# Kernel tuning notes

Hardware: AMD Instinct MI355X
Metric: run time of the kernel (lower is better)

The kernel has to match this reference:

```python
import jax, jax.numpy as jnp
import numpy as np


def _chamfer(xyz1, xyz2):
    # xyz1: [B,N,3], xyz2: [B,M,3]
    sq1 = jnp.sum(xyz1 * xyz1, axis=-1)               # [B,N]
    sq2 = jnp.sum(xyz2 * xyz2, axis=-1)               # [B,M]
    cross = jnp.einsum('bnc,bmc->bnm', xyz1, xyz2)    # [B,N,M]
    d = sq1[:, :, None] + sq2[:, None, :] - 2.0 * cross  # [B,N,M] squared dists
    dist1 = jnp.min(d, axis=2)                        # [B,N]
    idx1 = jnp.argmin(d, axis=2).astype(jnp.int32)    # [B,N]
    dist2 = jnp.min(d, axis=1)                        # [B,M]
    idx2 = jnp.argmin(d, axis=1).astype(jnp.int32)    # [B,M]
    return dist1, dist2, idx1, idx2


def setup_inputs() -> dict:
    key = jax.random.key(0)
    k1, k2 = jax.random.split(key)
    B, N, M = 2, 8192, 8192
    xyz1 = jax.random.normal(k1, (B, N, 3), dtype=jnp.float32)
    xyz2 = jax.random.normal(k2, (B, M, 3), dtype=jnp.float32)
    return {"xyz1": xyz1, "xyz2": xyz2}


def reference(xyz1, xyz2):
    # Matches ChamferDistanceFunction.forward: returns (dist1, dist2, idx1, idx2)
    # with SQUARED distances, as in the CUDA kernel.
    return _chamfer(xyz1, xyz2)
```

## Files before the change

kernel.cpp:

```cpp
#include <hip/hip_runtime.h>
#include <stdint.h>

#define TPB   256
#define Q     4
#define CHUNK 128

typedef unsigned long long ull;

__device__ __forceinline__ uint32_t enc_f32(float f) {
    uint32_t u = __float_as_uint(f);
    return (u & 0x80000000u) ? ~u : (u | 0x80000000u);
}

__device__ __forceinline__ float sq_np(float x, float y, float z) {
    return __fadd_rn(__fadd_rn(__fmul_rn(x, x), __fmul_rn(y, y)), __fmul_rn(z, z));
}

__global__ void __launch_bounds__(TPB) chamfer_pass1(
    const float* __restrict__ xyz1, const float* __restrict__ xyz2,
    ull* __restrict__ P, int B, int N, int M)
{
    __shared__ float4 pts[CHUNK];

    int z   = blockIdx.z;
    int dir = z / B;
    int b   = z - dir * B;

    const float* src; const float* dst; int Ns, Nd; size_t ebase;
    if (dir == 0) { src = xyz1; dst = xyz2; Ns = N; Nd = M; ebase = (size_t)b * N; }
    else          { src = xyz2; dst = xyz1; Ns = M; Nd = N; ebase = (size_t)B * N + (size_t)b * M; }

    int t     = threadIdx.x;
    int mbase = blockIdx.y * CHUNK;

    for (int i = t; i < CHUNK; i += TPB) {
        int m = mbase + i;
        if (m < Nd) {
            const float* p = dst + ((size_t)b * Nd + m) * 3;
            float x = p[0], y = p[1], zz = p[2];
            pts[i] = make_float4(x, y, zz, sq_np(x, y, zz));
        } else {
            pts[i] = make_float4(0.f, 0.f, 0.f, 3.0e38f);
        }
    }

    int n0 = blockIdx.x * (TPB * Q) + t;
    float qx[Q], qy[Q], qz[Q], qs[Q];
    #pragma unroll
    for (int k = 0; k < Q; ++k) {
        int n = n0 + k * TPB;
        if (n < Ns) {
            const float* p = src + ((size_t)b * Ns + n) * 3;
            qx[k] = p[0]; qy[k] = p[1]; qz[k] = p[2];
            qs[k] = sq_np(qx[k], qy[k], qz[k]);
        } else { qx[k] = 0.f; qy[k] = 0.f; qz[k] = 0.f; qs[k] = 0.f; }
    }
    __syncthreads();

    float best[Q];
    int   bidx[Q];
    #pragma unroll
    for (int k = 0; k < Q; ++k) { best[k] = 3.4e38f; bidx[k] = 0; }

    #pragma unroll 2
    for (int i = 0; i < CHUNK; i += 2) {
        float4 c0 = pts[i];
        float4 c1 = pts[i + 1];
        #pragma unroll
        for (int k = 0; k < Q; ++k) {
            float cr0 = __fadd_rn(__fadd_rn(__fmul_rn(qx[k], c0.x), __fmul_rn(qy[k], c0.y)),
                                  __fmul_rn(qz[k], c0.z));
            float d0  = fmaf(-2.0f, cr0, __fadd_rn(qs[k], c0.w));
            float cr1 = __fadd_rn(__fadd_rn(__fmul_rn(qx[k], c1.x), __fmul_rn(qy[k], c1.y)),
                                  __fmul_rn(qz[k], c1.z));
            float d1  = fmaf(-2.0f, cr1, __fadd_rn(qs[k], c1.w));
            float nb  = fminf(best[k], fminf(d0, d1));
            int   sel = (d0 == nb) ? (mbase + i) : (mbase + i + 1);
            bidx[k]   = (best[k] == nb) ? bidx[k] : sel;
            best[k]   = nb;
        }
    }

    #pragma unroll
    for (int k = 0; k < Q; ++k) {
        int n = n0 + k * TPB;
        if (n < Ns) {
            ull key = ((ull)enc_f32(best[k]) << 32) | (unsigned int)bidx[k];
            atomicMin(&P[ebase + n], key);
        }
    }
}

__global__ void __launch_bounds__(256) chamfer_unpack(
    const ull* __restrict__ P, float* __restrict__ out, int entries)
{
    int e = blockIdx.x * 256 + threadIdx.x;
    if (e < entries) {
        ull pk = P[e];
        uint32_t encu = (uint32_t)(pk >> 32);
        uint32_t bits = (encu & 0x80000000u) ? (encu & 0x7FFFFFFFu) : ~encu;
        out[e]           = __uint_as_float(bits);
        out[entries + e] = (float)(uint32_t)pk;
    }
}

__global__ void __launch_bounds__(1024) chamfer_unpack_inplace(float* __restrict__ out)
{
    const int entries = 32768;
    const ull* P = (const ull*)out;
    int t = threadIdx.x;
    ull v[32];
    #pragma unroll
    for (int k = 0; k < 32; ++k) v[k] = P[t + k * 1024];
    __syncthreads();
    #pragma unroll
    for (int k = 0; k < 32; ++k) {
        int e = t + k * 1024;
        ull pk = v[k];
        uint32_t encu = (uint32_t)(pk >> 32);
        uint32_t bits = (encu & 0x80000000u) ? (encu & 0x7FFFFFFFu) : ~encu;
        out[e]           = __uint_as_float(bits);
        out[entries + e] = (float)(uint32_t)pk;
    }
}

extern "C" void kernel_launch(void* const* d_in, const int* in_sizes, int n_in,
                              void* d_out, int out_size, void* d_ws, size_t ws_size,
                              hipStream_t stream) {
    const float* xyz1 = (const float*)d_in[0];
    const float* xyz2 = (const float*)d_in[1];
    const int B = 2;
    const int N = in_sizes[0] / (B * 3);
    const int M = in_sizes[1] / (B * 3);

    float* out = (float*)d_out;
    const int entries = B * N + B * M;
    const size_t pbytes = (size_t)entries * sizeof(ull);

    int maxP = (N > M) ? N : M;
    dim3 grid((maxP + TPB * Q - 1) / (TPB * Q), (maxP + CHUNK - 1) / CHUNK, 2 * B);

    if (ws_size >= pbytes) {
        ull* P = (ull*)d_ws;
        hipMemsetAsync(d_ws, 0xFF, pbytes, stream);
        chamfer_pass1<<<grid, TPB, 0, stream>>>(xyz1, xyz2, P, B, N, M);
        chamfer_unpack<<<(entries + 255) / 256, 256, 0, stream>>>(P, out, entries);
    } else {
        ull* P = (ull*)d_out;
        hipMemsetAsync(d_out, 0xFF, pbytes, stream);
        chamfer_pass1<<<grid, TPB, 0, stream>>>(xyz1, xyz2, P, B, N, M);
        if (entries == 32768) {
            chamfer_unpack_inplace<<<1, 1024, 0, stream>>>(out);
        } else {
            chamfer_unpack<<<1, 1, 0, stream>>>((const ull*)d_out, out, 0);
        }
    }
}
```

Before: 116.0 us.

## Fuse both chamfer directions into one tiled kernel with shared distance matrix

Replaces the two-direction launch, which computed every pairwise distance twice, with a single kernel. Each block computes a 64x64 distance tile once into shared memory, then reduces it along rows and along columns, using the row results for dist1 and the column results for dist2. This halves the distance arithmetic. In exchange it adds shared-memory stores and loads, extra barriers per chunk, and per-chunk atomics on the column side.

Measured after the change: 122.8 us. +5.8%, slower.

```diff
diff --git a/kernel.cpp b/kernel.cpp
--- a/kernel.cpp
+++ b/kernel.cpp
@@ -1,9 +1,11 @@
 #include <hip/hip_runtime.h>
 #include <stdint.h>
 
-#define TPB   256
-#define Q     4
-#define CHUNK 128
+#define TPB    256
+#define TR     64
+#define TC     64
+#define DSTR   65
+#define NCHK   16
 
 typedef unsigned long long ull;
 
@@ -16,78 +18,110 @@
     return __fadd_rn(__fadd_rn(__fmul_rn(x, x), __fmul_rn(y, y)), __fmul_rn(z, z));
 }
 
-__global__ void __launch_bounds__(TPB) chamfer_pass1(
+__global__ void __launch_bounds__(TPB) chamfer_fused(
     const float* __restrict__ xyz1, const float* __restrict__ xyz2,
     ull* __restrict__ P, int B, int N, int M)
 {
-    __shared__ float4 pts[CHUNK];
+    __shared__ float4 pts[TC];
+    __shared__ float  dmat[TR * DSTR];
+    __shared__ ull    mrg[4][TR];
 
-    int z   = blockIdx.z;
-    int dir = z / B;
-    int b   = z - dir * B;
+    int b = blockIdx.z;
+    int t = threadIdx.x;
+    int rbase  = blockIdx.x * TR;
+    int cbase0 = blockIdx.y * (TC * NCHK);
 
-    const float* src; const float* dst; int Ns, Nd; size_t ebase;
-    if (dir == 0) { src = xyz1; dst = xyz2; Ns = N; Nd = M; ebase = (size_t)b * N; }
-    else          { src = xyz2; dst = xyz1; Ns = M; Nd = N; ebase = (size_t)B * N + (size_t)b * M; }
+    int rq = t & 15;
+    int cq = t >> 4;
+    float ax[4], ay[4], az[4], aw[4];
+    #pragma unroll
+    for (int i = 0; i < 4; ++i) {
+        int n = rbase + rq * 4 + i;
+        if (n < N) {
+            const float* p = xyz1 + ((size_t)b * N + n) * 3;
+            ax[i] = p[0]; ay[i] = p[1]; az[i] = p[2];
+            aw[i] = sq_np(ax[i], ay[i], az[i]);
+        } else { ax[i] = 0.f; ay[i] = 0.f; az[i] = 0.f; aw[i] = 3.0e38f; }
+    }
 
-    int t     = threadIdx.x;
-    int mbase = blockIdx.y * CHUNK;
+    int rrow = t & 63;
+    int rseg = t >> 6;
+    float rbest = 3.4e38f; int rbcol = 0;
 
-    for (int i = t; i < CHUNK; i += TPB) {
-        int m = mbase + i;
-        if (m < Nd) {
-            const float* p = dst + ((size_t)b * Nd + m) * 3;
-            float x = p[0], y = p[1], zz = p[2];
-            pts[i] = make_float4(x, y, zz, sq_np(x, y, zz));
-        } else {
-            pts[i] = make_float4(0.f, 0.f, 0.f, 3.0e38f);
+    for (int ch = 0; ch < NCHK; ++ch) {
+        int cb = cbase0 + ch * TC;
+        __syncthreads();
+        if (t < TC) {
+            int m = cb + t;
+            if (m < M) {
+                const float* p = xyz2 + ((size_t)b * M + m) * 3;
+                float x = p[0], y = p[1], z = p[2];
+                pts[t] = make_float4(x, y, z, sq_np(x, y, z));
+            } else pts[t] = make_float4(0.f, 0.f, 0.f, 3.0e38f);
+        }
+        __syncthreads();
+
+        {
+            float dv[4][4];
+            #pragma unroll
+            for (int j = 0; j < 4; ++j) {
+                float4 c = pts[cq * 4 + j];
+                #pragma unroll
+                for (int i = 0; i < 4; ++i) {
+                    float cr = __fadd_rn(__fadd_rn(__fmul_rn(ax[i], c.x), __fmul_rn(ay[i], c.y)),
+                                         __fmul_rn(az[i], c.z));
+                    float s  = __fadd_rn(aw[i], c.w);
+                    dv[i][j] = fmaf(-2.0f, cr, s);
+                }
+            }
+            #pragma unroll
+            for (int i = 0; i < 4; ++i)
+                #pragma unroll
+                for (int j = 0; j < 4; ++j)
+                    dmat[(rq * 4 + i) * DSTR + cq * 4 + j] = dv[i][j];
+        }
+        __syncthreads();
+
+        {
+            const float* dr = &dmat[rrow * DSTR + rseg * 16];
+            #pragma unroll
+            for (int i = 0; i < 16; ++i) {
+                float d = dr[i];
+                if (d < rbest) { rbest = d; rbcol = cb + rseg * 16 + i; }
+            }
+        }
+
+        {
+            int ccol = t & 63, cseg = t >> 6;
+            float cbest = 3.4e38f; int cbrow = 0;
+            #pragma unroll
+            for (int i = 0; i < 16; ++i) {
+                float d = dmat[(cseg * 16 + i) * DSTR + ccol];
+                if (d < cbest) { cbest = d; cbrow = rbase + cseg * 16 + i; }
+            }
+            mrg[cseg][ccol] = ((ull)enc_f32(cbest) << 32) | (unsigned)cbrow;
+        }
+        __syncthreads();
+        if (t < TC) {
+            int m = cb + t;
+            ull k0 = mrg[0][t], k1 = mrg[1][t], k2 = mrg[2][t], k3 = mrg[3][t];
+            if (k1 < k0) k0 = k1;
+            if (k2 < k0) k0 = k2;
+            if (k3 < k0) k0 = k3;
+            if (m < M) atomicMin(&P[(size_t)B * N + (size_t)b * M + m], k0);
         }
     }
 
-    int n0 = blockIdx.x * (TPB * Q) + t;
-    float qx[Q], qy[Q], qz[Q], qs[Q];
-    #pragma unroll
-    for (int k = 0; k < Q; ++k) {
-        int n = n0 + k * TPB;
-        if (n < Ns) {
-            const float* p = src + ((size_t)b * Ns + n) * 3;
-            qx[k] = p[0]; qy[k] = p[1]; qz[k] = p[2];
-            qs[k] = sq_np(qx[k], qy[k], qz[k]);
-        } else { qx[k] = 0.f; qy[k] = 0.f; qz[k] = 0.f; qs[k] = 0.f; }
-    }
     __syncthreads();
-
-    float best[Q];
-    int   bidx[Q];
-    #pragma unroll
-    for (int k = 0; k < Q; ++k) { best[k] = 3.4e38f; bidx[k] = 0; }
-
-    #pragma unroll 2
-    for (int i = 0; i < CHUNK; i += 2) {
-        float4 c0 = pts[i];
-        float4 c1 = pts[i + 1];
-        #pragma unroll
-        for (int k = 0; k < Q; ++k) {
-            float cr0 = __fadd_rn(__fadd_rn(__fmul_rn(qx[k], c0.x), __fmul_rn(qy[k], c0.y)),
-                                  __fmul_rn(qz[k], c0.z));
-            float d0  = fmaf(-2.0f, cr0, __fadd_rn(qs[k], c0.w));
-            float cr1 = __fadd_rn(__fadd_rn(__fmul_rn(qx[k], c1.x), __fmul_rn(qy[k], c1.y)),
-                                  __fmul_rn(qz[k], c1.z));
-            float d1  = fmaf(-2.0f, cr1, __fadd_rn(qs[k], c1.w));
-            float nb  = fminf(best[k], fminf(d0, d1));
-            int   sel = (d0 == nb) ? (mbase + i) : (mbase + i + 1);
-            bidx[k]   = (best[k] == nb) ? bidx[k] : sel;
-            best[k]   = nb;
-        }
-    }
-
-    #pragma unroll
-    for (int k = 0; k < Q; ++k) {
-        int n = n0 + k * TPB;
-        if (n < Ns) {
-            ull key = ((ull)enc_f32(best[k]) << 32) | (unsigned int)bidx[k];
-            atomicMin(&P[ebase + n], key);
-        }
+    mrg[rseg][rrow] = ((ull)enc_f32(rbest) << 32) | (unsigned)rbcol;
+    __syncthreads();
+    if (t < TR) {
+        int n = rbase + t;
+        ull k0 = mrg[0][t], k1 = mrg[1][t], k2 = mrg[2][t], k3 = mrg[3][t];
+        if (k1 < k0) k0 = k1;
+        if (k2 < k0) k0 = k2;
+        if (k3 < k0) k0 = k3;
+        if (n < N) atomicMin(&P[(size_t)b * N + n], k0);
     }
 }
 
@@ -137,18 +171,17 @@
     const int entries = B * N + B * M;
     const size_t pbytes = (size_t)entries * sizeof(ull);
 
-    int maxP = (N > M) ? N : M;
-    dim3 grid((maxP + TPB * Q - 1) / (TPB * Q), (maxP + CHUNK - 1) / CHUNK, 2 * B);
+    dim3 grid((N + TR - 1) / TR, (M + TC * NCHK - 1) / (TC * NCHK), B);
 
     if (ws_size >= pbytes) {
         ull* P = (ull*)d_ws;
         hipMemsetAsync(d_ws, 0xFF, pbytes, stream);
-        chamfer_pass1<<<grid, TPB, 0, stream>>>(xyz1, xyz2, P, B, N, M);
+        chamfer_fused<<<grid, TPB, 0, stream>>>(xyz1, xyz2, P, B, N, M);
         chamfer_unpack<<<(entries + 255) / 256, 256, 0, stream>>>(P, out, entries);
     } else {
         ull* P = (ull*)d_out;
         hipMemsetAsync(d_out, 0xFF, pbytes, stream);
-        chamfer_pass1<<<grid, TPB, 0, stream>>>(xyz1, xyz2, P, B, N, M);
+        chamfer_fused<<<grid, TPB, 0, stream>>>(xyz1, xyz2, P, B, N, M);
         if (entries == 32768) {
             chamfer_unpack_inplace<<<1, 1024, 0, stream>>>(out);
         } else {
```
